# Performance work log

Hardware: AMD Instinct MI355X
Metric: run time of the kernel (lower is better)

## Reference

```python
import jax, jax.numpy as jnp
import numpy as np

N_HEADS = 16
HEAD_DIM = 128  # d_model // n_heads


def rope(x):
    # x: [B, H, T, D]. Matches the torch module: interleaved even/odd split,
    # then concat([x1*cos - x2*sin, x1*sin + x2*cos], axis=-1).
    T, D = x.shape[2], x.shape[3]
    inv_freq = 1.0 / (10000.0 ** (jnp.arange(0, D, 2, dtype=x.dtype) / D))  # [D/2]
    freqs = jnp.arange(T, dtype=x.dtype)[:, None] * inv_freq[None, :]       # [T, D/2]
    sin, cos = jnp.sin(freqs), jnp.cos(freqs)                               # [T, D/2]
    x1, x2 = x[..., ::2], x[..., 1::2]                                      # [B,H,T,D/2]
    return jnp.concatenate([x1 * cos - x2 * sin, x1 * sin + x2 * cos], axis=-1)


def setup_inputs() -> dict:
    key = jax.random.key(0)
    ks = jax.random.split(key, 5)
    B, T, C = 2, 2048, 2048
    scale = 1.0 / np.sqrt(C)
    return {
        "x": jax.random.normal(ks[0], (B, T, C), dtype=jnp.float32),
        "W_qkv": jax.random.normal(ks[1], (3 * C, C), dtype=jnp.float32) * scale,
        "b_qkv": jnp.zeros((3 * C,), dtype=jnp.float32),
        "W_out": jax.random.normal(ks[2], (C, C), dtype=jnp.float32) * scale,
        "b_out": jnp.zeros((C,), dtype=jnp.float32),
    }


def reference(x, W_qkv, b_qkv, W_out, b_out):
    B, T, C = x.shape
    H, D = N_HEADS, HEAD_DIM
    qkv = x @ W_qkv.T + b_qkv                      # [B, T, 3C]
    qkv = qkv.reshape(B, T, 3, H, D)
    q, k, v = qkv[:, :, 0], qkv[:, :, 1], qkv[:, :, 2]  # [B, T, H, D]
    q = rope(jnp.transpose(q, (0, 2, 1, 3)))       # [B, H, T, D]
    k = rope(jnp.transpose(k, (0, 2, 1, 3)))
    v = jnp.transpose(v, (0, 2, 1, 3))
    scores = jnp.einsum("bhqd,bhkd->bhqk", q, k) / jnp.sqrt(jnp.asarray(D, x.dtype))
    causal = jnp.tril(jnp.ones((T, T), dtype=bool))
    scores = jnp.where(causal, scores, jnp.finfo(x.dtype).min)
    attn = jax.nn.softmax(scores, axis=-1)
    out = jnp.einsum("bhqk,bhkd->bhqd", attn, v)   # [B, H, T, D]
    out = jnp.transpose(out, (0, 2, 1, 3)).reshape(B, T, C)
    return out @ W_out.T + b_out
```

## Files before the change

### kernel.cpp

```cpp
#include <hip/hip_runtime.h>
#include <hip/hip_bf16.h>

typedef __attribute__((ext_vector_type(8))) short bf16x8;
typedef __attribute__((ext_vector_type(4))) float f32x4;

#define GLOAD_LDS16(gptr, lptr) \
  __builtin_amdgcn_global_load_lds((const __attribute__((address_space(1))) void*)(gptr), \
                                   (__attribute__((address_space(3))) void*)(lptr), 16, 0, 0)

__device__ __forceinline__ unsigned short f2b(float f) {
  union { float f; unsigned u; } x; x.f = f;
  unsigned r = x.u + 0x7fffu + ((x.u >> 16) & 1u);
  return (unsigned short)(r >> 16);
}
__device__ __forceinline__ float b2f(unsigned short u) {
  union { unsigned u; float f; } x; x.u = ((unsigned)u) << 16;
  return x.f;
}

__global__ void cast_kernel(const float* __restrict__ in, unsigned short* __restrict__ out, int n) {
  const int i = (blockIdx.x * 256 + threadIdx.x) * 4;
  if (i < n) {
    const float4 v = *(const float4*)(in + i);
    ushort4 r;
    r.x = f2b(v.x); r.y = f2b(v.y); r.z = f2b(v.z); r.w = f2b(v.w);
    *(ushort4*)(out + i) = r;
  }
}

template<int OUTF32>
__global__ __launch_bounds__(512, 4)
void gemm128(const unsigned short* __restrict__ A,
             const unsigned short* __restrict__ Bm,
             const float* __restrict__ bias,
             void* __restrict__ Cp,
             int M, int N, int K)
{
  __shared__ __align__(16) char Lds[73728];
  const int t  = threadIdx.x;
  const int l  = t & 63;
  const int w  = t >> 6;
  const int lr = l & 15;
  const int lkb = (l >> 4) << 4;
  const int wr = w >> 2;
  const int wc = w & 3;

  const int nwg = gridDim.x;
  const int wg  = (blockIdx.x & 7) * (nwg >> 3) + (blockIdx.x >> 3);
  const int NBN = N >> 8;
  const int bm = wg / NBN, bn = wg % NBN;

  const long K2 = (long)K * 2;
  const char* Ab = (const char*)A  + (long)(bm * 128) * K2;
  const char* Bb = (const char*)Bm + (long)(bn * 256) * K2;

  auto swz = [](int a) -> int { return a ^ (((a >> 7) & 3) << 4); };

  const int t16 = t << 4;
  const int da  = swz(t16);
  const long sa = (long)(da >> 6) * K2 + (da & 63);
  const int db0 = swz(t16), db1 = swz(8192 + t16);
  const long sb0 = (long)(db0 >> 6) * K2 + (db0 & 63);
  const long sb1 = (long)(db1 >> 6) * K2 + (db1 & 63);

  auto stage = [&](int g) {
    char* S = Lds + (g % 3) * 24576;
    const char* As = Ab + (long)g * 64;
    const char* Bs = Bb + (long)g * 64;
    GLOAD_LDS16(As + sa,  S + t16);
    GLOAD_LDS16(Bs + sb0, S + 8192 + t16);
    GLOAD_LDS16(Bs + sb1, S + 16384 + t16);
  };

  int aoff[4], boff[4];
#pragma unroll
  for (int mi = 0; mi < 4; ++mi) {
    const int a = ((wr * 64 + mi * 16 + lr) << 6) | lkb;
    aoff[mi] = swz(a);
  }
#pragma unroll
  for (int ni = 0; ni < 4; ++ni) {
    const int a = ((wc * 64 + ni * 16 + lr) << 6) | lkb;
    boff[ni] = 8192 + swz(a);
  }

  f32x4 acc[4][4] = {};
  const int NT = K >> 5;
  bf16x8 af[4], bfr[4];

  stage(0); stage(1);
  asm volatile("s_waitcnt vmcnt(3)" ::: "memory");
  __builtin_amdgcn_s_barrier();
  __builtin_amdgcn_sched_barrier(0);
#pragma unroll
  for (int mi = 0; mi < 4; ++mi) af[mi]  = *(const bf16x8*)(Lds + aoff[mi]);
#pragma unroll
  for (int ni = 0; ni < 4; ++ni) bfr[ni] = *(const bf16x8*)(Lds + boff[ni]);

  for (int tt = 0; tt < NT; ++tt) {
    if (tt + 2 < NT) stage(tt + 2);
    __builtin_amdgcn_s_setprio(1);
#pragma unroll
    for (int mi = 0; mi < 4; ++mi)
#pragma unroll
      for (int ni = 0; ni < 4; ++ni)
        acc[mi][ni] = __builtin_amdgcn_mfma_f32_16x16x32_bf16(af[mi], bfr[ni], acc[mi][ni], 0, 0, 0);
    __builtin_amdgcn_s_setprio(0);
    if (tt + 1 < NT) {
      if (tt + 2 < NT) asm volatile("s_waitcnt vmcnt(3)" ::: "memory");
      else             asm volatile("s_waitcnt vmcnt(0)" ::: "memory");
      __builtin_amdgcn_s_barrier();
      __builtin_amdgcn_sched_barrier(0);
      const char* S = Lds + ((tt + 1) % 3) * 24576;
#pragma unroll
      for (int mi = 0; mi < 4; ++mi) af[mi]  = *(const bf16x8*)(S + aoff[mi]);
#pragma unroll
      for (int ni = 0; ni < 4; ++ni) bfr[ni] = *(const bf16x8*)(S + boff[ni]);
    }
  }

  const int roff = (l >> 4) << 2;
  const int row0 = bm * 128 + wr * 64 + roff;
  const int col0 = bn * 256 + wc * 64 + lr;
  float bv[4];
#pragma unroll
  for (int ni = 0; ni < 4; ++ni) bv[ni] = bias ? bias[col0 + ni * 16] : 0.0f;
#pragma unroll
  for (int mi = 0; mi < 4; ++mi) {
#pragma unroll
    for (int r = 0; r < 4; ++r) {
      const long rb = (long)(row0 + mi * 16 + r) * N;
#pragma unroll
      for (int ni = 0; ni < 4; ++ni) {
        const float v = acc[mi][ni][r] + bv[ni];
        if (OUTF32) ((float*)Cp)[rb + col0 + ni * 16] = v;
        else ((unsigned short*)Cp)[rb + col0 + ni * 16] = f2b(v);
      }
    }
  }
}

__global__ void prep_kernel(const unsigned short* __restrict__ qkv,
                            unsigned short* __restrict__ Qr,
                            unsigned short* __restrict__ Kr,
                            unsigned short* __restrict__ Vt)
{
  const int T = 2048;
  __shared__ unsigned short ld[128][65];
  const int bh = blockIdx.y, tb = blockIdx.x;
  const int b = bh >> 4, h = bh & 15;
  const int t = threadIdx.x;

#pragma unroll
  for (int i = 0; i < 16; ++i) {
    const int idx = i * 256 + t;
    const int d  = idx & 63;
    const int tt = tb * 64 + (idx >> 6);
    const long base = ((long)(b * T + tt) * 3) * 2048 + h * 128;
    const float inv = exp2f(-(float)d * 0.2076205059304602f);
    const float fr = (float)tt * inv;
    float sn, cs;
    sincosf(fr, &sn, &cs);
    const float q1 = b2f(qkv[base + 2 * d]);
    const float q2 = b2f(qkv[base + 2 * d + 1]);
    const float k1 = b2f(qkv[base + 2048 + 2 * d]);
    const float k2 = b2f(qkv[base + 2048 + 2 * d + 1]);
    const long ob = ((long)bh * T + tt) * 128;
    Qr[ob + d]      = f2b(q1 * cs - q2 * sn);
    Qr[ob + 64 + d] = f2b(q1 * sn + q2 * cs);
    Kr[ob + d]      = f2b(k1 * cs - k2 * sn);
    Kr[ob + 64 + d] = f2b(k1 * sn + k2 * cs);
  }

#pragma unroll
  for (int i = 0; i < 32; ++i) {
    const int idx = i * 256 + t;
    const int d = idx & 127, tr = idx >> 7;
    ld[d][tr] = qkv[((long)(b * T + tb * 64 + tr) * 3 + 2) * 2048 + h * 128 + d];
  }
  __syncthreads();
#pragma unroll
  for (int i = 0; i < 32; ++i) {
    const int idx = i * 256 + t;
    const int tc = idx & 63, dr = idx >> 6;
    Vt[((long)bh * 128 + dr) * T + tb * 64 + tc] = ld[dr][tc];
  }
}

__global__ __launch_bounds__(256)
void attn_fwd(const unsigned short* __restrict__ Q,
              const unsigned short* __restrict__ Kg,
              const unsigned short* __restrict__ Vt,
              unsigned short* __restrict__ O, int T)
{
  __shared__ __align__(16) unsigned short Ks[2][64 * 128];
  __shared__ __align__(16) unsigned short Vs[2][128 * 64];
  __shared__ __align__(16) unsigned short Ps[4][16 * 64];
  const int t = threadIdx.x;
  const int w = t >> 6, l = t & 63;
  const int lr = l & 15;
  const int g16 = (l >> 4) << 4;
  const int sw = (lr & 7) << 4;
  const int bh = blockIdx.x;
  const int qt = (gridDim.y - 1) - blockIdx.y;
  const int q0 = qt * 64 + w * 16;
  const long hbase = (long)bh * T * 128;
  const long hbase2 = hbase * 2;
  const long T2 = (long)T * 2;
  const int roff = (l >> 4) << 2;
  const float C1 = 0.08838834764831845f * 1.4426950408889634f;

  bf16x8 qf[4];
  const unsigned short* Qrow = Q + hbase + (long)(q0 + lr) * 128;
#pragma unroll
  for (int ds = 0; ds < 4; ++ds) qf[ds] = *(const bf16x8*)&Qrow[ds * 32 + (g16 >> 1)];

  f32x4 o[8] = {};
  float m[4]    = {-INFINITY, -INFINITY, -INFINITY, -INFINITY};
  float lsum[4] = {0.f, 0.f, 0.f, 0.f};

  auto stage = [&](int kt, int buf) {
#pragma unroll
    for (int c = 0; c < 4; ++c) {
      const int o2 = t * 16 + c * 4096;
      const int krow = o2 >> 8, kcb = o2 & 255;
      GLOAD_LDS16((const char*)Kg + hbase2 + (long)kt * 16384 + krow * 256 + (kcb ^ ((krow & 7) << 4)),
                  (char*)Ks[buf] + o2);
      const int vrow = o2 >> 7, vcb = o2 & 127;
      GLOAD_LDS16((const char*)Vt + (long)(bh * 128 + vrow) * T2 + (long)kt * 128 + (vcb ^ ((vrow & 7) << 4)),
                  (char*)Vs[buf] + o2);
    }
  };

  const int ntile = qt + 1;
  stage(0, 0);
  __syncthreads();

  for (int kt = 0; kt < ntile; ++kt) {
    const int cur = kt & 1;
    if (kt + 1 < ntile) stage(kt + 1, cur ^ 1);

    const char* KsB = (const char*)Ks[cur];
    const char* VsB = (const char*)Vs[cur];

    f32x4 s[4] = {};
    __builtin_amdgcn_s_setprio(1);
#pragma unroll
    for (int tj = 0; tj < 4; ++tj)
#pragma unroll
      for (int ds = 0; ds < 4; ++ds) {
        bf16x8 kf = *(const bf16x8*)(KsB + (tj * 16 + lr) * 256 + ((ds * 64 + g16) ^ sw));
        s[tj] = __builtin_amdgcn_mfma_f32_16x16x32_bf16(qf[ds], kf, s[tj], 0, 0, 0);
      }
    __builtin_amdgcn_s_setprio(0);

    if (kt == qt) {
#pragma unroll
      for (int tj = 0; tj < 4; ++tj)
#pragma unroll
        for (int j = 0; j < 4; ++j)
          if (kt * 64 + tj * 16 + lr > q0 + roff + j) s[tj][j] = -INFINITY;
    }

    float corr[4];
#pragma unroll
    for (int j = 0; j < 4; ++j) {
      float v = fmaxf(fmaxf(s[0][j], s[1][j]), fmaxf(s[2][j], s[3][j]));
      v = fmaxf(v, __shfl_xor(v, 1, 64));
      v = fmaxf(v, __shfl_xor(v, 2, 64));
      v = fmaxf(v, __shfl_xor(v, 4, 64));
      v = fmaxf(v, __shfl_xor(v, 8, 64));
      const float mn = fmaxf(m[j], v * C1);
      corr[j] = exp2f(m[j] - mn);
      m[j] = mn;
    }
    float rs[4] = {0.f, 0.f, 0.f, 0.f};
#pragma unroll
    for (int tj = 0; tj < 4; ++tj)
#pragma unroll
      for (int j = 0; j < 4; ++j) {
        const float p = exp2f(fmaf(s[tj][j], C1, -m[j]));
        rs[j] += p;
        const int prow = roff + j;
        *(unsigned short*)((char*)Ps[w] + prow * 128 + (((tj * 16 + lr) * 2) ^ ((prow & 7) << 4))) = f2b(p);
      }
#pragma unroll
    for (int j = 0; j < 4; ++j) {
      float v = rs[j];
      v += __shfl_xor(v, 1, 64);
      v += __shfl_xor(v, 2, 64);
      v += __shfl_xor(v, 4, 64);
      v += __shfl_xor(v, 8, 64);
      lsum[j] = lsum[j] * corr[j] + v;
    }
#pragma unroll
    for (int nj = 0; nj < 8; ++nj)
#pragma unroll
      for (int j = 0; j < 4; ++j) o[nj][j] *= corr[j];

    __builtin_amdgcn_s_setprio(1);
#pragma unroll
    for (int ks = 0; ks < 2; ++ks) {
      bf16x8 pf = *(const bf16x8*)((const char*)Ps[w] + lr * 128 + ((ks * 64 + g16) ^ sw));
#pragma unroll
      for (int nj = 0; nj < 8; ++nj) {
        bf16x8 vf = *(const bf16x8*)(VsB + (nj * 16 + lr) * 128 + ((ks * 64 + g16) ^ sw));
        o[nj] = __builtin_amdgcn_mfma_f32_16x16x32_bf16(pf, vf, o[nj], 0, 0, 0);
      }
    }
    __builtin_amdgcn_s_setprio(0);
    __syncthreads();
  }

  float inv[4];
#pragma unroll
  for (int j = 0; j < 4; ++j) inv[j] = 1.0f / lsum[j];
  const int b = bh >> 4, h = bh & 15;
#pragma unroll
  for (int nj = 0; nj < 8; ++nj)
#pragma unroll
    for (int j = 0; j < 4; ++j) {
      const int q = q0 + roff + j;
      const int d = nj * 16 + lr;
      O[(long)(b * T + q) * 2048 + h * 128 + d] = f2b(o[nj][j] * inv[j]);
    }
}

extern "C" void kernel_launch(void* const* d_in, const int* in_sizes, int n_in,
                              void* d_out, int out_size, void* d_ws, size_t ws_size,
                              hipStream_t stream)
{
  const int B = 2, T = 2048, C = 2048;
  const int M = B * T;
  const int N1 = 3 * C;
  const float* x    = (const float*)d_in[0];
  const float* Wqkv = (const float*)d_in[1];
  const float* bqkv = (const float*)d_in[2];
  const float* Wout = (const float*)d_in[3];
  const float* bout = (const float*)d_in[4];
  float* out = (float*)d_out;

  char* p = (char*)d_ws;
  unsigned short* xb    = (unsigned short*)p; p += (size_t)M * C * 2;
  unsigned short* wqkvb = (unsigned short*)p; p += (size_t)N1 * C * 2;
  unsigned short* woutb = (unsigned short*)p; p += (size_t)C * C * 2;
  unsigned short* qkv   = (unsigned short*)p; p += (size_t)M * N1 * 2;
  unsigned short* Qr    = (unsigned short*)p; p += (size_t)M * C * 2;
  unsigned short* Kr    = (unsigned short*)p; p += (size_t)M * C * 2;
  unsigned short* Vt    = (unsigned short*)p; p += (size_t)M * C * 2;
  unsigned short* Ob    = xb;

  cast_kernel<<<M * C / 1024, 256, 0, stream>>>(x, xb, M * C);
  cast_kernel<<<N1 * C / 1024, 256, 0, stream>>>(Wqkv, wqkvb, N1 * C);
  cast_kernel<<<C * C / 1024, 256, 0, stream>>>(Wout, woutb, C * C);

  gemm128<0><<<dim3((M / 128) * (N1 / 256)), 512, 0, stream>>>(xb, wqkvb, bqkv, qkv, M, N1, C);

  prep_kernel<<<dim3(T / 64, 32), 256, 0, stream>>>(qkv, Qr, Kr, Vt);

  attn_fwd<<<dim3(32, T / 64), 256, 0, stream>>>(Qr, Kr, Vt, Ob, T);

  gemm128<1><<<dim3((M / 128) * (C / 256)), 512, 0, stream>>>(Ob, woutb, bout, out, M, C, C);
}
```

Measured before the change: 307.5 us.

## Compute transposed S in attention and pass P through registers instead of LDS

The QK^T MFMA operands are swapped so each lane holds one query row's scores. Row max and row sum then need only two cross-lane shuffles instead of four per row, each lane keeps a single m and lsum, and the causal mask is adjusted to the transposed layout. The P matrix is packed to bf16 with v_cvt_pk_bf16_f32 and rearranged into the PV MFMA A-operand layout with lane shuffles, removing the per-wave Ps LDS buffer and its scalar stores and vector reads. In exchange it adds __shfl traffic (ds_bpermute) for P, the correction factors and the final normalisation, and relies on the hand-derived lane mapping being correct.

```diff
diff --git a/kernel.cpp b/kernel.cpp
--- a/kernel.cpp
+++ b/kernel.cpp
@@ -16,6 +16,11 @@
 __device__ __forceinline__ float b2f(unsigned short u) {
   union { unsigned u; float f; } x; x.u = ((unsigned)u) << 16;
   return x.f;
+}
+__device__ __forceinline__ unsigned cvt_pk_bf16(float lo, float hi) {
+  unsigned d;
+  asm("v_cvt_pk_bf16_f32 %0, %1, %2" : "=v"(d) : "v"(lo), "v"(hi));
+  return d;
 }
 
 __global__ void cast_kernel(const float* __restrict__ in, unsigned short* __restrict__ out, int n) {
@@ -195,11 +200,11 @@
 {
   __shared__ __align__(16) unsigned short Ks[2][64 * 128];
   __shared__ __align__(16) unsigned short Vs[2][128 * 64];
-  __shared__ __align__(16) unsigned short Ps[4][16 * 64];
   const int t = threadIdx.x;
   const int w = t >> 6, l = t & 63;
   const int lr = l & 15;
-  const int g16 = (l >> 4) << 4;
+  const int g  = l >> 4;
+  const int g16 = g << 4;
   const int sw = (lr & 7) << 4;
   const int bh = blockIdx.x;
   const int qt = (gridDim.y - 1) - blockIdx.y;
@@ -207,7 +212,7 @@
   const long hbase = (long)bh * T * 128;
   const long hbase2 = hbase * 2;
   const long T2 = (long)T * 2;
-  const int roff = (l >> 4) << 2;
+  const int roff = g << 2;
   const float C1 = 0.08838834764831845f * 1.4426950408889634f;
 
   bf16x8 qf[4];
@@ -216,8 +221,7 @@
   for (int ds = 0; ds < 4; ++ds) qf[ds] = *(const bf16x8*)&Qrow[ds * 32 + (g16 >> 1)];
 
   f32x4 o[8] = {};
-  float m[4]    = {-INFINITY, -INFINITY, -INFINITY, -INFINITY};
-  float lsum[4] = {0.f, 0.f, 0.f, 0.f};
+  float m = -INFINITY, lsum = 0.f;
 
   auto stage = [&](int kt, int buf) {
 #pragma unroll
@@ -250,7 +254,7 @@
 #pragma unroll
       for (int ds = 0; ds < 4; ++ds) {
         bf16x8 kf = *(const bf16x8*)(KsB + (tj * 16 + lr) * 256 + ((ds * 64 + g16) ^ sw));
-        s[tj] = __builtin_amdgcn_mfma_f32_16x16x32_bf16(qf[ds], kf, s[tj], 0, 0, 0);
+        s[tj] = __builtin_amdgcn_mfma_f32_16x16x32_bf16(kf, qf[ds], s[tj], 0, 0, 0);
       }
     __builtin_amdgcn_s_setprio(0);
 
@@ -258,63 +262,75 @@
 #pragma unroll
       for (int tj = 0; tj < 4; ++tj)
 #pragma unroll
-        for (int j = 0; j < 4; ++j)
-          if (kt * 64 + tj * 16 + lr > q0 + roff + j) s[tj][j] = -INFINITY;
-    }
-
-    float corr[4];
-#pragma unroll
-    for (int j = 0; j < 4; ++j) {
-      float v = fmaxf(fmaxf(s[0][j], s[1][j]), fmaxf(s[2][j], s[3][j]));
-      v = fmaxf(v, __shfl_xor(v, 1, 64));
-      v = fmaxf(v, __shfl_xor(v, 2, 64));
-      v = fmaxf(v, __shfl_xor(v, 4, 64));
-      v = fmaxf(v, __shfl_xor(v, 8, 64));
-      const float mn = fmaxf(m[j], v * C1);
-      corr[j] = exp2f(m[j] - mn);
-      m[j] = mn;
-    }
-    float rs[4] = {0.f, 0.f, 0.f, 0.f};
+        for (int r = 0; r < 4; ++r)
+          if (kt * 64 + tj * 16 + 4 * g + r > q0 + lr) s[tj][r] = -INFINITY;
+    }
+
+    float pmax = -INFINITY;
 #pragma unroll
     for (int tj = 0; tj < 4; ++tj)
 #pragma unroll
-      for (int j = 0; j < 4; ++j) {
-        const float p = exp2f(fmaf(s[tj][j], C1, -m[j]));
-        rs[j] += p;
-        const int prow = roff + j;
-        *(unsigned short*)((char*)Ps[w] + prow * 128 + (((tj * 16 + lr) * 2) ^ ((prow & 7) << 4))) = f2b(p);
-      }
-#pragma unroll
-    for (int j = 0; j < 4; ++j) {
-      float v = rs[j];
-      v += __shfl_xor(v, 1, 64);
-      v += __shfl_xor(v, 2, 64);
-      v += __shfl_xor(v, 4, 64);
-      v += __shfl_xor(v, 8, 64);
-      lsum[j] = lsum[j] * corr[j] + v;
-    }
+      for (int r = 0; r < 4; ++r) pmax = fmaxf(pmax, s[tj][r]);
+    pmax = fmaxf(pmax, __shfl_xor(pmax, 16, 64));
+    pmax = fmaxf(pmax, __shfl_xor(pmax, 32, 64));
+    const float mn = fmaxf(m, pmax * C1);
+    const float corr = exp2f(m - mn);
+    m = mn;
+
+    float p[4][4];
+    float rs = 0.f;
+#pragma unroll
+    for (int tj = 0; tj < 4; ++tj)
+#pragma unroll
+      for (int r = 0; r < 4; ++r) {
+        const float pv = exp2f(fmaf(s[tj][r], C1, -mn));
+        p[tj][r] = pv;
+        rs += pv;
+      }
+    rs += __shfl_xor(rs, 16, 64);
+    rs += __shfl_xor(rs, 32, 64);
+    lsum = lsum * corr + rs;
+
+    unsigned D8[4][2];
+#pragma unroll
+    for (int tj = 0; tj < 4; ++tj) {
+      D8[tj][0] = cvt_pk_bf16(p[tj][0], p[tj][1]);
+      D8[tj][1] = cvt_pk_bf16(p[tj][2], p[tj][3]);
+    }
+
+    float corrj[4];
+#pragma unroll
+    for (int j = 0; j < 4; ++j) corrj[j] = __shfl(corr, roff + j, 64);
 #pragma unroll
     for (int nj = 0; nj < 8; ++nj)
 #pragma unroll
-      for (int j = 0; j < 4; ++j) o[nj][j] *= corr[j];
+      for (int j = 0; j < 4; ++j) o[nj][j] *= corrj[j];
 
     __builtin_amdgcn_s_setprio(1);
 #pragma unroll
     for (int ks = 0; ks < 2; ++ks) {
-      bf16x8 pf = *(const bf16x8*)((const char*)Ps[w] + lr * 128 + ((ks * 64 + g16) ^ sw));
+      union { unsigned u[4]; bf16x8 v; } pfu;
+#pragma unroll
+      for (int k2 = 0; k2 < 4; ++k2) {
+        const int src = lr | ((2 * (g & 1) + (k2 >> 1)) << 4);
+        const unsigned dwA = __shfl(D8[2 * ks][k2 & 1], src, 64);
+        const unsigned dwB = __shfl(D8[2 * ks + 1][k2 & 1], src, 64);
+        pfu.u[k2] = (g & 2) ? dwB : dwA;
+      }
 #pragma unroll
       for (int nj = 0; nj < 8; ++nj) {
         bf16x8 vf = *(const bf16x8*)(VsB + (nj * 16 + lr) * 128 + ((ks * 64 + g16) ^ sw));
-        o[nj] = __builtin_amdgcn_mfma_f32_16x16x32_bf16(pf, vf, o[nj], 0, 0, 0);
+        o[nj] = __builtin_amdgcn_mfma_f32_16x16x32_bf16(pfu.v, vf, o[nj], 0, 0, 0);
       }
     }
     __builtin_amdgcn_s_setprio(0);
     __syncthreads();
   }
 
-  float inv[4];
-#pragma unroll
-  for (int j = 0; j < 4; ++j) inv[j] = 1.0f / lsum[j];
+  const float inv = 1.0f / lsum;
+  float invj[4];
+#pragma unroll
+  for (int j = 0; j < 4; ++j) invj[j] = __shfl(inv, roff + j, 64);
   const int b = bh >> 4, h = bh & 15;
 #pragma unroll
   for (int nj = 0; nj < 8; ++nj)
@@ -322,7 +338,7 @@
     for (int j = 0; j < 4; ++j) {
       const int q = q0 + roff + j;
       const int d = nj * 16 + lr;
-      O[(long)(b * T + q) * 2048 + h * 128 + d] = f2b(o[nj][j] * inv[j]);
+      O[(long)(b * T + q) * 2048 + h * 128 + d] = f2b(o[nj][j] * invj[j]);
     }
 }
 
```

New measurement: 290.8 us. 1.06x faster.
